# Kernel optimization log

Hardware: AMD Instinct MI355X
Metric: run time of the kernel (lower is better)

The kernel has to match this reference:

```python
import jax, jax.numpy as jnp
import numpy as np

B, S, D = 4, 2048, 1024
DFF = 4 * D
NE = 4        # routed experts
NS = 2        # shared experts
TOPK = 2
CAP_F = 1.25


def _gelu(v):
    return jax.nn.gelu(v, approximate=False)  # torch nn.GELU default (erf)


def setup_inputs() -> dict:
    key = jax.random.key(0)
    ks = jax.random.split(key, 9)
    s = 0.02
    f = lambda k, sh: jax.random.normal(k, sh, dtype=jnp.float32) * s
    return {
        "hidden_states": jax.random.normal(ks[0], (B, S, D), dtype=jnp.float32),
        "router_w1": f(ks[1], (D, D)), "router_b1": jnp.zeros((D,), jnp.float32),
        "router_w2": f(ks[2], (D, NE)), "router_b2": jnp.zeros((NE,), jnp.float32),
        "re_w1": f(ks[3], (NE, D, DFF)), "re_b1": jnp.zeros((NE, DFF), jnp.float32),
        "re_w2": f(ks[4], (NE, DFF, D)), "re_b2": jnp.zeros((NE, D), jnp.float32),
        "se_w1": f(ks[5], (NS, D, DFF)), "se_b1": jnp.zeros((NS, DFF), jnp.float32),
        "se_w2": f(ks[6], (NS, DFF, D)), "se_b2": jnp.zeros((NS, D), jnp.float32),
        "out_w": f(ks[7], (D, D)), "out_b": jnp.zeros((D,), jnp.float32),
    }


def reference(hidden_states, router_w1, router_b1, router_w2, router_b2,
              re_w1, re_b1, re_w2, re_b2, se_w1, se_b1, se_w2, se_b2,
              out_w, out_b):
    b, s, d = hidden_states.shape
    T = b * s
    x = hidden_states.reshape(T, d)

    # --- router ---
    logits = _gelu(x @ router_w1 + router_b1) @ router_w2 + router_b2  # [T, NE]
    top_v, top_i = jax.lax.top_k(logits, TOPK)
    rweights = jax.nn.softmax(top_v, axis=-1)                          # [T, TOPK]
    z_loss = jnp.mean(jnp.square(jax.nn.logsumexp(logits, axis=-1)))

    capacity = int(T / NE * CAP_F)  # static Python int

    # padded token slot T absorbs dropped/overflow contributions, discarded later
    x_pad = jnp.concatenate([x, jnp.zeros((1, d), x.dtype)], axis=0)
    final = jnp.zeros((T + 1, d), x.dtype)

    for i in range(TOPK):
        eidx = top_i[:, i]
        w_pad = jnp.concatenate([rweights[:, i], jnp.zeros((1,), x.dtype)])
        for j in range(NE):
            # first `capacity` tokens routed to expert j (deterministic capacity drop)
            idx = jnp.nonzero(eidx == j, size=capacity, fill_value=T)[0]  # [capacity]
            h = _gelu(x_pad[idx] @ re_w1[j] + re_b1[j]) @ re_w2[j] + re_b2[j]
            final = final.at[idx].add(w_pad[idx][:, None] * h)
    final = final[:T]

    # shared experts (dense, weight 1/NS each)
    for j in range(NS):
        final = final + (1.0 / NS) * (_gelu(x @ se_w1[j] + se_b1[j]) @ se_w2[j] + se_b2[j])

    out = final @ out_w + out_b
    out = out * 0.5 + x * 0.5
    mu = jnp.mean(out, axis=-1, keepdims=True)
    var = jnp.var(out, axis=-1, keepdims=True)
    out = (out - mu) / jnp.sqrt(var + 1e-6)  # layer_norm, no affine, eps=1e-6
    return out.reshape(b, s, d), z_loss
```

## Files before the change

kernel.cpp:

```cpp
#include <hip/hip_runtime.h>
#include <hip/hip_bf16.h>
#include <math.h>

#define TTOK 8192
#define DM 1024
#define DFFN 4096
#define NEXP 4
#define CAPACITY 2560
#define EROWSN (2*CAPACITY)

typedef short bf16x8 __attribute__((ext_vector_type(8)));
typedef float f32x4 __attribute__((ext_vector_type(4)));

__device__ __forceinline__ unsigned short f2bf(float f) {
  unsigned int u = __float_as_uint(f);
  u = (u + 0x7fffu + ((u >> 16) & 1u)) >> 16;
  return (unsigned short)u;
}
__device__ __forceinline__ float bf2f(unsigned short h) {
  return __uint_as_float(((unsigned int)h) << 16);
}
__device__ __forceinline__ float gelu_f(float v) {
  float z = fabsf(v) * 0.7071067811865476f;
  float t = 1.0f / (1.0f + 0.3275911f * z);
  float p = t * (0.254829592f +
            t * (-0.284496736f +
            t * (1.421413741f +
            t * (-1.453152027f + t * 1.061405429f))));
  float er = 1.0f - p * __expf(-z * z);
  er = v >= 0.f ? er : -er;
  return 0.5f * v * (1.0f + er);
}
__device__ __forceinline__ void gl16(const void* g, void* l) {
  __builtin_amdgcn_global_load_lds((const __attribute__((address_space(1))) void*)g,
                                   (__attribute__((address_space(3))) void*)l, 16, 0, 0);
}

__global__ void k_cvt_x(const float* __restrict__ x, unsigned short* __restrict__ xhi,
                        unsigned short* __restrict__ xlo) {
  int i = blockIdx.x * blockDim.x + threadIdx.x;
  const int n4 = (TTOK + 1) * DM / 4;
  if (i >= n4) return;
  int base = i * 4;
  float v[4] = {0.f, 0.f, 0.f, 0.f};
  if (base < TTOK * DM) {
    float4 f = *reinterpret_cast<const float4*>(x + base);
    v[0] = f.x; v[1] = f.y; v[2] = f.z; v[3] = f.w;
  }
  ushort4 h, l;
  unsigned short hh[4], ll[4];
#pragma unroll
  for (int j = 0; j < 4; j++) {
    hh[j] = f2bf(v[j]);
    ll[j] = f2bf(v[j] - bf2f(hh[j]));
  }
  h.x = hh[0]; h.y = hh[1]; h.z = hh[2]; h.w = hh[3];
  l.x = ll[0]; l.y = ll[1]; l.z = ll[2]; l.w = ll[3];
  reinterpret_cast<ushort4*>(xhi)[i] = h;
  reinterpret_cast<ushort4*>(xlo)[i] = l;
}

__global__ void k_tcvt(const float* __restrict__ W, unsigned short* __restrict__ Wt,
                       int K, int N) {
  __shared__ float tile[32][33];
  int tx = threadIdx.x, ty = threadIdx.y;
  int n0 = blockIdx.x * 32, k0 = blockIdx.y * 32;
#pragma unroll
  for (int i = 0; i < 4; i++)
    tile[ty + i * 8][tx] = W[(size_t)(k0 + ty + i * 8) * N + n0 + tx];
  __syncthreads();
#pragma unroll
  for (int i = 0; i < 4; i++)
    Wt[(size_t)(n0 + ty + i * 8) * K + k0 + tx] = f2bf(tile[tx][ty + i * 8]);
}

__global__ void k_tcvt2(const float* __restrict__ W, unsigned short* __restrict__ Whi,
                        unsigned short* __restrict__ Wlo, int K, int N) {
  __shared__ float tile[32][33];
  int tx = threadIdx.x, ty = threadIdx.y;
  int n0 = blockIdx.x * 32, k0 = blockIdx.y * 32;
#pragma unroll
  for (int i = 0; i < 4; i++)
    tile[ty + i * 8][tx] = W[(size_t)(k0 + ty + i * 8) * N + n0 + tx];
  __syncthreads();
#pragma unroll
  for (int i = 0; i < 4; i++) {
    float v = tile[tx][ty + i * 8];
    unsigned short h = f2bf(v);
    Whi[(size_t)(n0 + ty + i * 8) * K + k0 + tx] = h;
    Wlo[(size_t)(n0 + ty + i * 8) * K + k0 + tx] = f2bf(v - bf2f(h));
  }
}

__global__ __launch_bounds__(256) void k_router(
    const unsigned short* __restrict__ xhi, const unsigned short* __restrict__ xlo,
    const unsigned short* __restrict__ whi, const unsigned short* __restrict__ wlo,
    const float* __restrict__ bias, float* __restrict__ Hr) {
  const int t = threadIdx.x;
  const int m0 = blockIdx.y * 128, n0 = blockIdx.x * 128;
  __shared__ unsigned short sAh[2][4096], sAl[2][4096], sBh[2][4096], sBl[2][4096];
  const int offA0 = t * 16, offA1 = offA0 + 4096;
  const int i0 = offA0 >> 1, i1 = offA1 >> 1;
  const int r0 = offA0 >> 6, c0e = (offA0 & 63) >> 1;
  const int r1 = offA1 >> 6, c1e = (offA1 & 63) >> 1;
  const unsigned short* pAh0 = xhi + (size_t)(m0 + r0) * DM + c0e;
  const unsigned short* pAh1 = xhi + (size_t)(m0 + r1) * DM + c1e;
  const unsigned short* pAl0 = xlo + (size_t)(m0 + r0) * DM + c0e;
  const unsigned short* pAl1 = xlo + (size_t)(m0 + r1) * DM + c1e;
  const unsigned short* pBh0 = whi + (size_t)(n0 + r0) * DM + c0e;
  const unsigned short* pBh1 = whi + (size_t)(n0 + r1) * DM + c1e;
  const unsigned short* pBl0 = wlo + (size_t)(n0 + r0) * DM + c0e;
  const unsigned short* pBl1 = wlo + (size_t)(n0 + r1) * DM + c1e;
  const int lane = t & 63, wid = t >> 6;
  const int wm = (wid >> 1) * 64, wn = (wid & 1) * 64;
  const int fr = lane & 15, fk = (lane >> 4) * 8;
  f32x4 acc[4][4];
#pragma unroll
  for (int m = 0; m < 4; m++)
#pragma unroll
    for (int n = 0; n < 4; n++) acc[m][n] = (f32x4){0.f, 0.f, 0.f, 0.f};

  auto stage = [&](int b, int k) {
    gl16(pAh0 + k, &sAh[b][i0]); gl16(pAh1 + k, &sAh[b][i1]);
    gl16(pAl0 + k, &sAl[b][i0]); gl16(pAl1 + k, &sAl[b][i1]);
    gl16(pBh0 + k, &sBh[b][i0]); gl16(pBh1 + k, &sBh[b][i1]);
    gl16(pBl0 + k, &sBl[b][i0]); gl16(pBl1 + k, &sBl[b][i1]);
  };

  int cur = 0;
  stage(0, 0);
  __syncthreads();
  for (int k0 = 0; k0 < DM; k0 += 32) {
    if (k0 + 32 < DM) stage(cur ^ 1, k0 + 32);
    bf16x8 ah[4], al[4], bh[4], bl[4];
#pragma unroll
    for (int m = 0; m < 4; m++) {
      ah[m] = *reinterpret_cast<const bf16x8*>(&sAh[cur][(wm + m * 16 + fr) * 32 + fk]);
      al[m] = *reinterpret_cast<const bf16x8*>(&sAl[cur][(wm + m * 16 + fr) * 32 + fk]);
    }
#pragma unroll
    for (int n = 0; n < 4; n++) {
      bh[n] = *reinterpret_cast<const bf16x8*>(&sBh[cur][(wn + n * 16 + fr) * 32 + fk]);
      bl[n] = *reinterpret_cast<const bf16x8*>(&sBl[cur][(wn + n * 16 + fr) * 32 + fk]);
    }
#pragma unroll
    for (int m = 0; m < 4; m++)
#pragma unroll
      for (int n = 0; n < 4; n++) {
        acc[m][n] = __builtin_amdgcn_mfma_f32_16x16x32_bf16(ah[m], bh[n], acc[m][n], 0, 0, 0);
        acc[m][n] = __builtin_amdgcn_mfma_f32_16x16x32_bf16(ah[m], bl[n], acc[m][n], 0, 0, 0);
        acc[m][n] = __builtin_amdgcn_mfma_f32_16x16x32_bf16(al[m], bh[n], acc[m][n], 0, 0, 0);
      }
    __syncthreads();
    cur ^= 1;
  }
  const int er = (lane >> 4) * 4, ec = lane & 15;
#pragma unroll
  for (int n = 0; n < 4; n++) {
    const int cc = n0 + wn + n * 16 + ec;
    const float bn = bias[cc];
#pragma unroll
    for (int m = 0; m < 4; m++) {
      const int rbase = m0 + wm + m * 16 + er;
#pragma unroll
      for (int j = 0; j < 4; j++)
        Hr[(size_t)(rbase + j) * DM + cc] = gelu_f(acc[m][n][j] + bn);
    }
  }
}

template <int MODE>
__global__ __launch_bounds__(512, 2) void k_gemm256(
    const unsigned short* __restrict__ A, const unsigned short* __restrict__ Bt,
    const float* __restrict__ bias, float* __restrict__ outF,
    unsigned short* __restrict__ outBf, const int* __restrict__ rows,
    const float* __restrict__ rwgt, const int* __restrict__ rowsPad,
    int N, int K, int klen) {
  if constexpr (MODE == 0 || MODE == 2) {
    if ((int)(blockIdx.y * 256) >= rowsPad[0]) return;
  }
  __shared__ unsigned short lds[65536];
  const int tid = threadIdx.x;
  const int lane = tid & 63, wid = tid >> 6;
  const int wr = wid >> 2, wc = wid & 3;
  const int fr = lane & 15;
  const int fkb = (lane >> 4) * 16;
  const int sw4 = (fr & 7) << 4;
  const int k0o = (fkb ^ sw4) >> 1;
  const int k1o = ((fkb + 64) ^ sw4) >> 1;
  const int m0 = blockIdx.y * 256, n0 = blockIdx.x * 256;
  int kbeg = 0;
  if constexpr (MODE == 2 || MODE == 3) kbeg = blockIdx.z * klen;
  const int nt = klen >> 6;

  const unsigned short *srcA[2][2], *srcB[2][2];
#pragma unroll
  for (int h = 0; h < 2; h++)
#pragma unroll
    for (int r = 0; r < 2; r++) {
      int d = h * 16384 + r * 8192 + tid * 16;
      int L = d ^ (((d >> 7) & 7) << 4);
      int row = L >> 7, k = (L & 127) >> 1;
      size_t arow;
      if constexpr (MODE == 0) arow = (size_t)rows[m0 + row];
      else arow = (size_t)(m0 + row);
      srcA[h][r] = A + arow * (size_t)K + kbeg + k;
      srcB[h][r] = Bt + (size_t)(n0 + row) * K + kbeg + k;
    }
  auto stA = [&](int buf, int h, int t) {
    unsigned short* d = lds + buf * 16384 + h * 8192 + tid * 8;
    gl16(srcA[h][0] + t * 64, d);
    gl16(srcA[h][1] + t * 64, d + 4096);
  };
  auto stB = [&](int buf, int h, int t) {
    unsigned short* d = lds + 32768 + buf * 16384 + h * 8192 + tid * 8;
    gl16(srcB[h][0] + t * 64, d);
    gl16(srcB[h][1] + t * 64, d + 4096);
  };

  f32x4 acc[8][4];
#pragma unroll
  for (int a = 0; a < 8; a++)
#pragma unroll
    for (int b = 0; b < 4; b++) acc[a][b] = (f32x4){0.f, 0.f, 0.f, 0.f};

  bf16x8 af0[4][2], af1[4][2], bf0[2][2], bf1[2][2];

  auto rdA = [&](bf16x8 (&dst)[4][2], int buf, int mh) {
    const unsigned short* Ab = lds + buf * 16384 + mh * 8192 + wr * 4096 + fr * 64;
#pragma unroll
    for (int m = 0; m < 4; m++) {
      dst[m][0] = *reinterpret_cast<const bf16x8*>(Ab + m * 1024 + k0o);
      dst[m][1] = *reinterpret_cast<const bf16x8*>(Ab + m * 1024 + k1o);
    }
  };
  auto rdB = [&](bf16x8 (&dst)[2][2], int buf, int nh) {
    const unsigned short* Bb = lds + 32768 + buf * 16384 + nh * 8192 + wc * 2048 + fr * 64;
#pragma unroll
    for (int n = 0; n < 2; n++) {
      dst[n][0] = *reinterpret_cast<const bf16x8*>(Bb + n * 1024 + k0o);
      dst[n][1] = *reinterpret_cast<const bf16x8*>(Bb + n * 1024 + k1o);
    }
  };
  auto mfmaQ = [&](bf16x8 (&a)[4][2], bf16x8 (&b)[2][2], int mh, int nh) {
    __builtin_amdgcn_s_setprio(1);
#pragma unroll
    for (int m = 0; m < 4; m++)
#pragma unroll
      for (int n = 0; n < 2; n++)
#pragma unroll
        for (int kk = 0; kk < 2; kk++)
          acc[mh * 4 + m][nh * 2 + n] = __builtin_amdgcn_mfma_f32_16x16x32_bf16(
              a[m][kk], b[n][kk], acc[mh * 4 + m][nh * 2 + n], 0, 0, 0);
    __builtin_amdgcn_s_setprio(0);
  };

#define BAR_PRE  do { __builtin_amdgcn_sched_barrier(0); __builtin_amdgcn_s_barrier();   \
                      asm volatile("s_waitcnt lgkmcnt(0)" ::: "memory");                 \
                      __builtin_amdgcn_sched_barrier(0); } while (0)
#define BAR_POST do { __builtin_amdgcn_sched_barrier(0); __builtin_amdgcn_s_barrier();   \
                      __builtin_amdgcn_sched_barrier(0); } while (0)
#define VM10 asm volatile("s_waitcnt vmcnt(10)" ::: "memory")
#define VM0  asm volatile("s_waitcnt vmcnt(0)" ::: "memory")

  stA(0, 0, 0); stB(0, 0, 0); stB(0, 1, 0); stA(0, 1, 0);
  stA(1, 0, 1); stB(1, 0, 1); stB(1, 1, 1);
  VM10;
  __builtin_amdgcn_s_barrier();
  __builtin_amdgcn_sched_barrier(0);

  for (int s = 0; s < nt - 2; ++s) {
    const int buf = s & 1;
    rdA(af0, buf, 0); rdB(bf0, buf, 0);
    stA(buf ^ 1, 1, s + 1);
    VM10; BAR_PRE; mfmaQ(af0, bf0, 0, 0); BAR_POST;
    rdB(bf1, buf, 1);
    stA(buf, 0, s + 2);
    VM10; BAR_PRE; mfmaQ(af0, bf1, 0, 1); BAR_POST;
    rdA(af1, buf, 1);
    stB(buf, 0, s + 2);
    BAR_PRE; mfmaQ(af1, bf1, 1, 1); BAR_POST;
    stB(buf, 1, s + 2);
    VM10; BAR_PRE; mfmaQ(af1, bf0, 1, 0); BAR_POST;
  }
  {
    const int buf = (nt - 2) & 1;
    rdA(af0, buf, 0); rdB(bf0, buf, 0);
    stA(buf ^ 1, 1, nt - 1);
    VM0; BAR_PRE; mfmaQ(af0, bf0, 0, 0); BAR_POST;
    rdB(bf1, buf, 1);
    BAR_PRE; mfmaQ(af0, bf1, 0, 1); BAR_POST;
    rdA(af1, buf, 1);
    BAR_PRE; mfmaQ(af1, bf1, 1, 1); BAR_POST;
    BAR_PRE; mfmaQ(af1, bf0, 1, 0); BAR_POST;
  }
  {
    const int buf = (nt - 1) & 1;
    rdA(af0, buf, 0); rdB(bf0, buf, 0);
    BAR_PRE; mfmaQ(af0, bf0, 0, 0); BAR_POST;
    rdB(bf1, buf, 1);
    BAR_PRE; mfmaQ(af0, bf1, 0, 1); BAR_POST;
    rdA(af1, buf, 1);
    BAR_PRE; mfmaQ(af1, bf1, 1, 1); BAR_POST;
    BAR_PRE; mfmaQ(af1, bf0, 1, 0); BAR_POST;
  }
#undef BAR_PRE
#undef BAR_POST
#undef VM10
#undef VM0

  const int er = (lane >> 4) * 4, ec = lane & 15;
  if constexpr (MODE <= 1) {
    unsigned short* cb = lds + wid * 8192;
#pragma unroll
    for (int b = 0; b < 4; b++) {
      const int nh = b >> 1, n = b & 1;
      const int cc = n0 + nh * 128 + wc * 32 + n * 16 + ec;
      const float bn = bias[cc];
      const int cl = nh * 32 + n * 16 + ec;
#pragma unroll
      for (int a = 0; a < 8; a++) {
        const int mh = a >> 2, m = a & 3;
#pragma unroll
        for (int j = 0; j < 4; j++) {
          int rl = mh * 64 + m * 16 + er + j;
          int addr = rl * 64 + ((((cl >> 3) ^ (rl & 7)) << 3) | (cl & 7));
          cb[addr] = f2bf(gelu_f(acc[a][b][j] + bn));
        }
      }
    }
#pragma unroll
    for (int it = 0; it < 16; it++) {
      int rl = it * 8 + (lane >> 3);
      int cblk = lane & 7;
      int laddr = rl * 64 + ((cblk ^ (rl & 7)) << 3);
      bf16x8 v = *reinterpret_cast<const bf16x8*>(cb + laddr);
      int grow = m0 + (rl >> 6) * 128 + wr * 64 + (rl & 63);
      int gcol = n0 + (cblk >> 2) * 128 + wc * 32 + (cblk & 3) * 8;
      *reinterpret_cast<bf16x8*>(outBf + (size_t)grow * N + gcol) = v;
    }
  } else {
    float bnz[4];
    int ccs[4];
#pragma unroll
    for (int b = 0; b < 4; b++) {
      ccs[b] = n0 + (b >> 1) * 128 + wc * 32 + (b & 1) * 16 + ec;
      if constexpr (MODE == 4) bnz[b] = bias[ccs[b]];
      else bnz[b] = (blockIdx.z == 0) ? bias[ccs[b]] : 0.f;
    }
#pragma unroll
    for (int a = 0; a < 8; a++) {
#pragma unroll
      for (int j = 0; j < 4; j++) {
        const int rr = m0 + (a >> 2) * 128 + wr * 64 + (a & 3) * 16 + er + j;
        if constexpr (MODE == 2) {
          const int tok = rows[rr];
          if (tok < TTOK) {
            const float w = rwgt[rr];
#pragma unroll
            for (int b = 0; b < 4; b++)
              atomicAdd(outF + (size_t)tok * DM + ccs[b], w * (acc[a][b][j] + bnz[b]));
          }
        } else if constexpr (MODE == 3) {
#pragma unroll
          for (int b = 0; b < 4; b++)
            atomicAdd(outF + (size_t)rr * DM + ccs[b], 0.5f * (acc[a][b][j] + bnz[b]));
        } else {
#pragma unroll
          for (int b = 0; b < 4; b++)
            outF[(size_t)rr * N + ccs[b]] = acc[a][b][j] + bnz[b];
        }
      }
    }
  }
}

__global__ __launch_bounds__(256) void k_logits(const float* __restrict__ Hr,
                                                const float* __restrict__ w2,
                                                const float* __restrict__ b2,
                                                float* __restrict__ logits) {
  int tok = blockIdx.x * 4 + (threadIdx.x >> 6);
  int lane = threadIdx.x & 63;
  const float* h = Hr + (size_t)tok * DM;
  float s0 = 0.f, s1 = 0.f, s2 = 0.f, s3 = 0.f;
  for (int d = lane; d < DM; d += 64) {
    float hv = h[d];
    s0 += hv * w2[d * 4 + 0];
    s1 += hv * w2[d * 4 + 1];
    s2 += hv * w2[d * 4 + 2];
    s3 += hv * w2[d * 4 + 3];
  }
#pragma unroll
  for (int off = 32; off >= 1; off >>= 1) {
    s0 += __shfl_down(s0, off, 64);
    s1 += __shfl_down(s1, off, 64);
    s2 += __shfl_down(s2, off, 64);
    s3 += __shfl_down(s3, off, 64);
  }
  if (lane == 0) {
    logits[tok * 4 + 0] = s0 + b2[0];
    logits[tok * 4 + 1] = s1 + b2[1];
    logits[tok * 4 + 2] = s2 + b2[2];
    logits[tok * 4 + 3] = s3 + b2[3];
  }
}

__global__ void k_topk(const float* __restrict__ logits, int* __restrict__ e0,
                       int* __restrict__ e1, float* __restrict__ w0,
                       float* __restrict__ w1, float* __restrict__ zout) {
  int tok = blockIdx.x * blockDim.x + threadIdx.x;
  if (tok >= TTOK) return;
  float l[4];
#pragma unroll
  for (int j = 0; j < 4; j++) l[j] = logits[tok * 4 + j];
  int i0 = 0; float v0 = l[0];
#pragma unroll
  for (int j = 1; j < 4; j++) if (l[j] > v0) { v0 = l[j]; i0 = j; }
  int i1 = -1; float v1 = -1e30f;
#pragma unroll
  for (int j = 0; j < 4; j++) if (j != i0 && l[j] > v1) { v1 = l[j]; i1 = j; }
  float d = expf(v1 - v0);
  float a = 1.f / (1.f + d);
  e0[tok] = i0; e1[tok] = i1;
  w0[tok] = a;  w1[tok] = d * a;
  float se = 0.f;
#pragma unroll
  for (int j = 0; j < 4; j++) se += expf(l[j] - v0);
  float lse = v0 + logf(se);
  atomicAdd(zout, lse * lse * (1.0f / TTOK));
}

__global__ __launch_bounds__(256) void k_lists(const int* __restrict__ e0,
                                               const int* __restrict__ e1,
                                               const float* __restrict__ w0,
                                               const float* __restrict__ w1,
                                               int* __restrict__ list,
                                               float* __restrict__ lwgt,
                                               int* __restrict__ cnt) {
  int b = blockIdx.x;
  int prio = b >> 2, j = b & 3;
  const int* e = prio ? e1 : e0;
  const float* w = prio ? w1 : w0;
  __shared__ int warpsum[4];
  __shared__ int sbase;
  if (threadIdx.x == 0) sbase = 0;
  __syncthreads();
  int lane = threadIdx.x & 63, wv = threadIdx.x >> 6;
  for (int t0 = 0; t0 < TTOK; t0 += 256) {
    int tok = t0 + threadIdx.x;
    bool p = (e[tok] == j);
    unsigned long long bal = __ballot(p);
    int pre = __popcll(bal & ((1ull << lane) - 1ull));
    if (lane == 0) warpsum[wv] = __popcll(bal);
    __syncthreads();
    int woff = 0;
    for (int q = 0; q < wv; q++) woff += warpsum[q];
    int tot = warpsum[0] + warpsum[1] + warpsum[2] + warpsum[3];
    int slot = sbase + woff + pre;
    if (p && slot < CAPACITY) {
      list[b * CAPACITY + slot] = tok;
      lwgt[b * CAPACITY + slot] = w[tok];
    }
    __syncthreads();
    if (threadIdx.x == 0) sbase += tot;
    __syncthreads();
  }
  if (threadIdx.x == 0) cnt[b] = min(sbase, CAPACITY);
}

__global__ void k_combine(const int* __restrict__ list, const float* __restrict__ lwgt,
                          const int* __restrict__ cnt, int* __restrict__ erows,
                          float* __restrict__ ewgt, int* __restrict__ rowsPad) {
  int j = blockIdx.x;
  int c0 = cnt[j], c1 = cnt[4 + j];
  for (int s = threadIdx.x; s < EROWSN; s += blockDim.x) {
    int tok = TTOK; float wv = 0.f;
    if (s < c0) { tok = list[j * CAPACITY + s]; wv = lwgt[j * CAPACITY + s]; }
    else if (s < c0 + c1) {
      tok = list[(4 + j) * CAPACITY + (s - c0)];
      wv = lwgt[(4 + j) * CAPACITY + (s - c0)];
    }
    erows[j * EROWSN + s] = tok;
    ewgt[j * EROWSN + s] = wv;
  }
  if (threadIdx.x == 0) rowsPad[j] = ((c0 + c1 + 255) / 256) * 256;
}

__global__ void k_cvt_final(const float* __restrict__ f, unsigned short* __restrict__ fb) {
  int i = blockIdx.x * blockDim.x + threadIdx.x;
  if (i >= TTOK * DM / 4) return;
  float4 v = reinterpret_cast<const float4*>(f)[i];
  ushort4 o;
  o.x = f2bf(v.x); o.y = f2bf(v.y); o.z = f2bf(v.z); o.w = f2bf(v.w);
  reinterpret_cast<ushort4*>(fb)[i] = o;
}

__global__ __launch_bounds__(256) void k_ln(const float* __restrict__ OUT,
                                            const float* __restrict__ x,
                                            float* __restrict__ out) {
  int r = blockIdx.x;
  const float* o = OUT + (size_t)r * DM;
  const float* xr = x + (size_t)r * DM;
  int t = threadIdx.x;
  float v[4];
  float s = 0.f, s2 = 0.f;
#pragma unroll
  for (int i = 0; i < 4; i++) {
    int d = t + i * 256;
    float val = 0.5f * o[d] + 0.5f * xr[d];
    v[i] = val; s += val; s2 += val * val;
  }
#pragma unroll
  for (int off = 32; off >= 1; off >>= 1) {
    s += __shfl_down(s, off, 64);
    s2 += __shfl_down(s2, off, 64);
  }
  __shared__ float rs[4], rs2[4];
  int wv = t >> 6, lane = t & 63;
  if (lane == 0) { rs[wv] = s; rs2[wv] = s2; }
  __syncthreads();
  s = rs[0] + rs[1] + rs[2] + rs[3];
  s2 = rs2[0] + rs2[1] + rs2[2] + rs2[3];
  float mu = s * (1.f / DM);
  float var = s2 * (1.f / DM) - mu * mu;
  float inv = 1.0f / sqrtf(var + 1e-6f);
#pragma unroll
  for (int i = 0; i < 4; i++)
    out[(size_t)r * DM + t + i * 256] = (v[i] - mu) * inv;
}

static constexpr size_t OFF_XHI = 0;
static constexpr size_t SZ_XHI = (size_t)(TTOK + 1) * DM * 2;
static constexpr size_t OFF_ACT = OFF_XHI + SZ_XHI;
static constexpr size_t SZ_ACT = (size_t)TTOK * DFFN * 2;
static constexpr size_t OFF_WBUF = OFF_ACT + SZ_ACT;
static constexpr size_t SZ_WBUF = (size_t)2 * DM * DFFN * 2;
static constexpr size_t OFF_FINAL = OFF_WBUF + SZ_WBUF;
static constexpr size_t SZ_FINAL = (size_t)TTOK * DM * 4;
static constexpr size_t OFF_MISC = OFF_FINAL + SZ_FINAL;
static constexpr size_t OFF_LOGITS = OFF_MISC;
static constexpr size_t OFF_E0 = OFF_LOGITS + (size_t)TTOK * 4 * 4;
static constexpr size_t OFF_E1 = OFF_E0 + (size_t)TTOK * 4;
static constexpr size_t OFF_W0 = OFF_E1 + (size_t)TTOK * 4;
static constexpr size_t OFF_W1 = OFF_W0 + (size_t)TTOK * 4;
static constexpr size_t OFF_LIST = OFF_W1 + (size_t)TTOK * 4;
static constexpr size_t OFF_LWGT = OFF_LIST + (size_t)8 * CAPACITY * 4;
static constexpr size_t OFF_CNT = OFF_LWGT + (size_t)8 * CAPACITY * 4;
static constexpr size_t OFF_EROWS = OFF_CNT + 64;
static constexpr size_t OFF_EWGT = OFF_EROWS + (size_t)NEXP * EROWSN * 4;
static constexpr size_t OFF_RPAD = OFF_EWGT + (size_t)NEXP * EROWSN * 4;

extern "C" void kernel_launch(void* const* d_in, const int* in_sizes, int n_in,
                              void* d_out, int out_size, void* d_ws, size_t ws_size,
                              hipStream_t stream) {
  const float* x = (const float*)d_in[0];
  const float* rw1 = (const float*)d_in[1];
  const float* rb1 = (const float*)d_in[2];
  const float* rw2 = (const float*)d_in[3];
  const float* rb2 = (const float*)d_in[4];
  const float* re_w1 = (const float*)d_in[5];
  const float* re_b1 = (const float*)d_in[6];
  const float* re_w2 = (const float*)d_in[7];
  const float* re_b2 = (const float*)d_in[8];
  const float* se_w1 = (const float*)d_in[9];
  const float* se_b1 = (const float*)d_in[10];
  const float* se_w2 = (const float*)d_in[11];
  const float* se_b2 = (const float*)d_in[12];
  const float* out_w = (const float*)d_in[13];
  const float* out_b = (const float*)d_in[14];
  float* outp = (float*)d_out;

  char* ws = (char*)d_ws;
  unsigned short* xhi = (unsigned short*)(ws + OFF_XHI);
  float* Hr = (float*)(ws + OFF_ACT);
  unsigned short* xlo = (unsigned short*)(ws + OFF_ACT + 33554432);
  unsigned short* act = (unsigned short*)(ws + OFF_ACT);
  unsigned short* fbf = (unsigned short*)(ws + OFF_ACT);
  float* OUTb = (float*)(ws + OFF_ACT + 16777216);
  unsigned short* w1t = (unsigned short*)(ws + OFF_WBUF);
  unsigned short* w2t = w1t + (size_t)DM * DFFN;
  unsigned short* rwhi = w1t;
  unsigned short* rwlo = w1t + (size_t)DM * DM;
  unsigned short* owt = w1t;
  float* finalb = (float*)(ws + OFF_FINAL);
  float* logits = (float*)(ws + OFF_LOGITS);
  int* e0 = (int*)(ws + OFF_E0);
  int* e1 = (int*)(ws + OFF_E1);
  float* w0 = (float*)(ws + OFF_W0);
  float* w1 = (float*)(ws + OFF_W1);
  int* list = (int*)(ws + OFF_LIST);
  float* lwgt = (float*)(ws + OFF_LWGT);
  int* cnt = (int*)(ws + OFF_CNT);
  int* erows = (int*)(ws + OFF_EROWS);
  float* ewgt = (float*)(ws + OFF_EWGT);
  int* rpad = (int*)(ws + OFF_RPAD);
  float* zout = outp + (size_t)TTOK * DM;

  hipMemsetAsync(finalb, 0, SZ_FINAL, stream);
  hipMemsetAsync(zout, 0, 4, stream);

  {
    int n4 = (TTOK + 1) * DM / 4;
    k_cvt_x<<<(n4 + 255) / 256, 256, 0, stream>>>(x, xhi, xlo);
  }
  k_tcvt2<<<dim3(DM / 32, DM / 32), dim3(32, 8), 0, stream>>>(rw1, rwhi, rwlo, DM, DM);
  k_router<<<dim3(DM / 128, TTOK / 128), 256, 0, stream>>>(xhi, xlo, rwhi, rwlo, rb1, Hr);
  k_logits<<<TTOK / 4, 256, 0, stream>>>(Hr, rw2, rb2, logits);
  k_topk<<<TTOK / 256, 256, 0, stream>>>(logits, e0, e1, w0, w1, zout);
  k_lists<<<8, 256, 0, stream>>>(e0, e1, w0, w1, list, lwgt, cnt);
  k_combine<<<NEXP, 256, 0, stream>>>(list, lwgt, cnt, erows, ewgt, rpad);

  for (int j = 0; j < NEXP; j++) {
    k_tcvt<<<dim3(DFFN / 32, DM / 32), dim3(32, 8), 0, stream>>>(
        re_w1 + (size_t)j * DM * DFFN, w1t, DM, DFFN);
    k_tcvt<<<dim3(DM / 32, DFFN / 32), dim3(32, 8), 0, stream>>>(
        re_w2 + (size_t)j * DFFN * DM, w2t, DFFN, DM);
    k_gemm256<0><<<dim3(DFFN / 256, EROWSN / 256), 512, 0, stream>>>(
        xhi, w1t, re_b1 + (size_t)j * DFFN, nullptr, act,
        erows + (size_t)j * EROWSN, nullptr, rpad + j, DFFN, DM, DM);
    k_gemm256<2><<<dim3(DM / 256, EROWSN / 256, 4), 512, 0, stream>>>(
        act, w2t, re_b2 + (size_t)j * DM, finalb, nullptr,
        erows + (size_t)j * EROWSN, ewgt + (size_t)j * EROWSN, rpad + j, DM, DFFN, 1024);
  }
  for (int j = 0; j < 2; j++) {
    k_tcvt<<<dim3(DFFN / 32, DM / 32), dim3(32, 8), 0, stream>>>(
        se_w1 + (size_t)j * DM * DFFN, w1t, DM, DFFN);
    k_tcvt<<<dim3(DM / 32, DFFN / 32), dim3(32, 8), 0, stream>>>(
        se_w2 + (size_t)j * DFFN * DM, w2t, DFFN, DM);
    k_gemm256<1><<<dim3(DFFN / 256, TTOK / 256), 512, 0, stream>>>(
        xhi, w1t, se_b1 + (size_t)j * DFFN, nullptr, act, nullptr, nullptr, nullptr,
        DFFN, DM, DM);
    k_gemm256<3><<<dim3(DM / 256, TTOK / 256, 2), 512, 0, stream>>>(
        act, w2t, se_b2 + (size_t)j * DM, finalb, nullptr, nullptr, nullptr, nullptr,
        DM, DFFN, 2048);
  }
  k_cvt_final<<<TTOK * DM / 4 / 256, 256, 0, stream>>>(finalb, fbf);
  k_tcvt<<<dim3(DM / 32, DM / 32), dim3(32, 8), 0, stream>>>(out_w, owt, DM, DM);
  k_gemm256<4><<<dim3(DM / 256, TTOK / 256), 512, 0, stream>>>(
      fbf, owt, out_b, OUTb, nullptr, nullptr, nullptr, nullptr, DM, DM, DM);
  k_ln<<<TTOK, 256, 0, stream>>>(OUTb, x, outp);
}
```

Baseline: 1.293 ms.

## Simplify GEMM pipeline, vectorize weight transpose, split-K output projection

Replaces the hand-scheduled GEMM main loop, which used quarter-step barriers, vmcnt waits and priority hints, with a plain double-buffered loop that loads the next tile, computes the whole tile and then syncs. It also drops the two-blocks-per-CU launch bound. The weight transpose-convert kernel now handles 64x32 tiles and writes 8 bf16 values per store. The output projection GEMM switches to split-K over two slices with atomicAdd into a zeroed buffer. Together these trade fine-grained load/compute overlap for simpler code, and add an extra memset plus atomic traffic on the output.

```diff
diff --git a/kernel.cpp b/kernel.cpp
--- a/kernel.cpp
+++ b/kernel.cpp
@@ -62,16 +62,19 @@
 
 __global__ void k_tcvt(const float* __restrict__ W, unsigned short* __restrict__ Wt,
                        int K, int N) {
-  __shared__ float tile[32][33];
+  __shared__ float tile[64][33];
   int tx = threadIdx.x, ty = threadIdx.y;
-  int n0 = blockIdx.x * 32, k0 = blockIdx.y * 32;
-#pragma unroll
-  for (int i = 0; i < 4; i++)
+  int n0 = blockIdx.x * 32, k0 = blockIdx.y * 64;
+#pragma unroll
+  for (int i = 0; i < 8; i++)
     tile[ty + i * 8][tx] = W[(size_t)(k0 + ty + i * 8) * N + n0 + tx];
   __syncthreads();
-#pragma unroll
-  for (int i = 0; i < 4; i++)
-    Wt[(size_t)(n0 + ty + i * 8) * K + k0 + tx] = f2bf(tile[tx][ty + i * 8]);
+  int t = ty * 32 + tx;
+  int n = t >> 3, ko = (t & 7) * 8;
+  bf16x8 v;
+#pragma unroll
+  for (int i = 0; i < 8; i++) v[i] = (short)f2bf(tile[ko + i][n]);
+  *reinterpret_cast<bf16x8*>(Wt + (size_t)(n0 + n) * K + k0 + ko) = v;
 }
 
 __global__ void k_tcvt2(const float* __restrict__ W, unsigned short* __restrict__ Whi,
@@ -170,7 +173,7 @@
 }
 
 template <int MODE>
-__global__ __launch_bounds__(512, 2) void k_gemm256(
+__global__ __launch_bounds__(512) void k_gemm256(
     const unsigned short* __restrict__ A, const unsigned short* __restrict__ Bt,
     const float* __restrict__ bias, float* __restrict__ outF,
     unsigned short* __restrict__ outBf, const int* __restrict__ rows,
@@ -190,7 +193,7 @@
   const int k1o = ((fkb + 64) ^ sw4) >> 1;
   const int m0 = blockIdx.y * 256, n0 = blockIdx.x * 256;
   int kbeg = 0;
-  if constexpr (MODE == 2 || MODE == 3) kbeg = blockIdx.z * klen;
+  if constexpr (MODE >= 2) kbeg = blockIdx.z * klen;
   const int nt = klen >> 6;
 
   const unsigned short *srcA[2][2], *srcB[2][2];
@@ -225,7 +228,6 @@
     for (int b = 0; b < 4; b++) acc[a][b] = (f32x4){0.f, 0.f, 0.f, 0.f};
 
   bf16x8 af0[4][2], af1[4][2], bf0[2][2], bf1[2][2];
-
   auto rdA = [&](bf16x8 (&dst)[4][2], int buf, int mh) {
     const unsigned short* Ab = lds + buf * 16384 + mh * 8192 + wr * 4096 + fr * 64;
 #pragma unroll
@@ -242,72 +244,41 @@
       dst[n][1] = *reinterpret_cast<const bf16x8*>(Bb + n * 1024 + k1o);
     }
   };
-  auto mfmaQ = [&](bf16x8 (&a)[4][2], bf16x8 (&b)[2][2], int mh, int nh) {
-    __builtin_amdgcn_s_setprio(1);
-#pragma unroll
-    for (int m = 0; m < 4; m++)
-#pragma unroll
-      for (int n = 0; n < 2; n++)
-#pragma unroll
-        for (int kk = 0; kk < 2; kk++)
-          acc[mh * 4 + m][nh * 2 + n] = __builtin_amdgcn_mfma_f32_16x16x32_bf16(
-              a[m][kk], b[n][kk], acc[mh * 4 + m][nh * 2 + n], 0, 0, 0);
-    __builtin_amdgcn_s_setprio(0);
-  };
-
-#define BAR_PRE  do { __builtin_amdgcn_sched_barrier(0); __builtin_amdgcn_s_barrier();   \
-                      asm volatile("s_waitcnt lgkmcnt(0)" ::: "memory");                 \
-                      __builtin_amdgcn_sched_barrier(0); } while (0)
-#define BAR_POST do { __builtin_amdgcn_sched_barrier(0); __builtin_amdgcn_s_barrier();   \
-                      __builtin_amdgcn_sched_barrier(0); } while (0)
-#define VM10 asm volatile("s_waitcnt vmcnt(10)" ::: "memory")
-#define VM0  asm volatile("s_waitcnt vmcnt(0)" ::: "memory")
-
-  stA(0, 0, 0); stB(0, 0, 0); stB(0, 1, 0); stA(0, 1, 0);
-  stA(1, 0, 1); stB(1, 0, 1); stB(1, 1, 1);
-  VM10;
-  __builtin_amdgcn_s_barrier();
-  __builtin_amdgcn_sched_barrier(0);
-
-  for (int s = 0; s < nt - 2; ++s) {
+
+  stA(0, 0, 0); stA(0, 1, 0); stB(0, 0, 0); stB(0, 1, 0);
+  __syncthreads();
+
+  for (int s = 0; s < nt; ++s) {
     const int buf = s & 1;
-    rdA(af0, buf, 0); rdB(bf0, buf, 0);
-    stA(buf ^ 1, 1, s + 1);
-    VM10; BAR_PRE; mfmaQ(af0, bf0, 0, 0); BAR_POST;
-    rdB(bf1, buf, 1);
-    stA(buf, 0, s + 2);
-    VM10; BAR_PRE; mfmaQ(af0, bf1, 0, 1); BAR_POST;
-    rdA(af1, buf, 1);
-    stB(buf, 0, s + 2);
-    BAR_PRE; mfmaQ(af1, bf1, 1, 1); BAR_POST;
-    stB(buf, 1, s + 2);
-    VM10; BAR_PRE; mfmaQ(af1, bf0, 1, 0); BAR_POST;
-  }
-  {
-    const int buf = (nt - 2) & 1;
-    rdA(af0, buf, 0); rdB(bf0, buf, 0);
-    stA(buf ^ 1, 1, nt - 1);
-    VM0; BAR_PRE; mfmaQ(af0, bf0, 0, 0); BAR_POST;
-    rdB(bf1, buf, 1);
-    BAR_PRE; mfmaQ(af0, bf1, 0, 1); BAR_POST;
-    rdA(af1, buf, 1);
-    BAR_PRE; mfmaQ(af1, bf1, 1, 1); BAR_POST;
-    BAR_PRE; mfmaQ(af1, bf0, 1, 0); BAR_POST;
-  }
-  {
-    const int buf = (nt - 1) & 1;
-    rdA(af0, buf, 0); rdB(bf0, buf, 0);
-    BAR_PRE; mfmaQ(af0, bf0, 0, 0); BAR_POST;
-    rdB(bf1, buf, 1);
-    BAR_PRE; mfmaQ(af0, bf1, 0, 1); BAR_POST;
-    rdA(af1, buf, 1);
-    BAR_PRE; mfmaQ(af1, bf1, 1, 1); BAR_POST;
-    BAR_PRE; mfmaQ(af1, bf0, 1, 0); BAR_POST;
-  }
-#undef BAR_PRE
-#undef BAR_POST
-#undef VM10
-#undef VM0
+    if (s + 1 < nt) {
+      stA(buf ^ 1, 0, s + 1); stA(buf ^ 1, 1, s + 1);
+      stB(buf ^ 1, 0, s + 1); stB(buf ^ 1, 1, s + 1);
+    }
+    rdA(af0, buf, 0); rdA(af1, buf, 1);
+    rdB(bf0, buf, 0); rdB(bf1, buf, 1);
+#pragma unroll
+    for (int kk = 0; kk < 2; kk++) {
+#pragma unroll
+      for (int m = 0; m < 4; m++) {
+#pragma unroll
+        for (int n = 0; n < 2; n++)
+          acc[m][n] = __builtin_amdgcn_mfma_f32_16x16x32_bf16(af0[m][kk], bf0[n][kk], acc[m][n], 0, 0, 0);
+#pragma unroll
+        for (int n = 0; n < 2; n++)
+          acc[m][2 + n] = __builtin_amdgcn_mfma_f32_16x16x32_bf16(af0[m][kk], bf1[n][kk], acc[m][2 + n], 0, 0, 0);
+      }
+#pragma unroll
+      for (int m = 0; m < 4; m++) {
+#pragma unroll
+        for (int n = 0; n < 2; n++)
+          acc[4 + m][n] = __builtin_amdgcn_mfma_f32_16x16x32_bf16(af1[m][kk], bf0[n][kk], acc[4 + m][n], 0, 0, 0);
+#pragma unroll
+        for (int n = 0; n < 2; n++)
+          acc[4 + m][2 + n] = __builtin_amdgcn_mfma_f32_16x16x32_bf16(af1[m][kk], bf1[n][kk], acc[4 + m][2 + n], 0, 0, 0);
+      }
+    }
+    __syncthreads();
+  }
 
   const int er = (lane >> 4) * 4, ec = lane & 15;
   if constexpr (MODE <= 1) {
@@ -345,8 +316,7 @@
 #pragma unroll
     for (int b = 0; b < 4; b++) {
       ccs[b] = n0 + (b >> 1) * 128 + wc * 32 + (b & 1) * 16 + ec;
-      if constexpr (MODE == 4) bnz[b] = bias[ccs[b]];
-      else bnz[b] = (blockIdx.z == 0) ? bias[ccs[b]] : 0.f;
+      bnz[b] = (blockIdx.z == 0) ? bias[ccs[b]] : 0.f;
     }
 #pragma unroll
     for (int a = 0; a < 8; a++) {
@@ -368,7 +338,7 @@
         } else {
 #pragma unroll
           for (int b = 0; b < 4; b++)
-            outF[(size_t)rr * N + ccs[b]] = acc[a][b][j] + bnz[b];
+            atomicAdd(outF + (size_t)rr * N + ccs[b], acc[a][b][j] + bnz[b]);
         }
       }
     }
@@ -611,9 +581,9 @@
   k_combine<<<NEXP, 256, 0, stream>>>(list, lwgt, cnt, erows, ewgt, rpad);
 
   for (int j = 0; j < NEXP; j++) {
-    k_tcvt<<<dim3(DFFN / 32, DM / 32), dim3(32, 8), 0, stream>>>(
+    k_tcvt<<<dim3(DFFN / 32, DM / 64), dim3(32, 8), 0, stream>>>(
         re_w1 + (size_t)j * DM * DFFN, w1t, DM, DFFN);
-    k_tcvt<<<dim3(DM / 32, DFFN / 32), dim3(32, 8), 0, stream>>>(
+    k_tcvt<<<dim3(DM / 32, DFFN / 64), dim3(32, 8), 0, stream>>>(
         re_w2 + (size_t)j * DFFN * DM, w2t, DFFN, DM);
     k_gemm256<0><<<dim3(DFFN / 256, EROWSN / 256), 512, 0, stream>>>(
         xhi, w1t, re_b1 + (size_t)j * DFFN, nullptr, act,
@@ -623,9 +593,9 @@
         erows + (size_t)j * EROWSN, ewgt + (size_t)j * EROWSN, rpad + j, DM, DFFN, 1024);
   }
   for (int j = 0; j < 2; j++) {
-    k_tcvt<<<dim3(DFFN / 32, DM / 32), dim3(32, 8), 0, stream>>>(
+    k_tcvt<<<dim3(DFFN / 32, DM / 64), dim3(32, 8), 0, stream>>>(
         se_w1 + (size_t)j * DM * DFFN, w1t, DM, DFFN);
-    k_tcvt<<<dim3(DM / 32, DFFN / 32), dim3(32, 8), 0, stream>>>(
+    k_tcvt<<<dim3(DM / 32, DFFN / 64), dim3(32, 8), 0, stream>>>(
         se_w2 + (size_t)j * DFFN * DM, w2t, DFFN, DM);
     k_gemm256<1><<<dim3(DFFN / 256, TTOK / 256), 512, 0, stream>>>(
         xhi, w1t, se_b1 + (size_t)j * DFFN, nullptr, act, nullptr, nullptr, nullptr,
@@ -635,8 +605,9 @@
         DM, DFFN, 2048);
   }
   k_cvt_final<<<TTOK * DM / 4 / 256, 256, 0, stream>>>(finalb, fbf);
-  k_tcvt<<<dim3(DM / 32, DM / 32), dim3(32, 8), 0, stream>>>(out_w, owt, DM, DM);
-  k_gemm256<4><<<dim3(DM / 256, TTOK / 256), 512, 0, stream>>>(
-      fbf, owt, out_b, OUTb, nullptr, nullptr, nullptr, nullptr, DM, DM, DM);
+  hipMemsetAsync(OUTb, 0, (size_t)TTOK * DM * 4, stream);
+  k_tcvt<<<dim3(DM / 32, DM / 64), dim3(32, 8), 0, stream>>>(out_w, owt, DM, DM);
+  k_gemm256<4><<<dim3(DM / 256, TTOK / 256, 2), 512, 0, stream>>>(
+      fbf, owt, out_b, OUTb, nullptr, nullptr, nullptr, nullptr, DM, DM, 512);
   k_ln<<<TTOK, 256, 0, stream>>>(OUTb, x, outp);
 }
```

After: 1.322 ms. 2.2% more time.
